# Performance work log

Measured on AMD Instinct MI355X. Metric: run time of the kernel, lower is better.

## Reference

```python
import jax, jax.numpy as jnp
import numpy as np

B, T, C, A, D, H, W = 2, 16, 64, 64, 32, 32, 32  # batch, timepoints, channels, att_features, spatial


def setup_inputs() -> dict:
    key = jax.random.key(0)
    ks = jax.random.split(key, 7)
    s = 1.0 / np.sqrt(C)
    return {
        "x": jax.random.normal(ks[0], (B, T, C, D, H, W), dtype=jnp.float32),
        "Wk": jax.random.normal(ks[1], (A, C), dtype=jnp.float32) * s,
        "bk": jax.random.normal(ks[2], (A,), dtype=jnp.float32) * s,
        "Wq": jax.random.normal(ks[3], (A, C), dtype=jnp.float32) * s,
        "bq": jax.random.normal(ks[4], (A,), dtype=jnp.float32) * s,
        "Wv": jax.random.normal(ks[5], (C, C), dtype=jnp.float32) * s,
        "bv": jax.random.normal(ks[6], (C,), dtype=jnp.float32) * s,
    }


def reference(x, Wk, bk, Wq, bq, Wv, bv):
    # kernel=1 Conv3d == pointwise channel mixing. Project and move spatial
    # dims to the front exactly like movedim((3,4,5),(1,2,3)):
    # result layout [B, D, H, W, T, out_ch].
    def proj(Wt, bt):
        return jnp.einsum('btcdhw,oc->bdhwto', x, Wt) + bt

    k = proj(Wk, bk)  # [B,D,H,W,T,A]
    q = proj(Wq, bq)  # [B,D,H,W,T,A]
    v = proj(Wv, bv)  # [B,D,H,W,T,C]

    scale = 1.0 / np.sqrt(float(Wk.shape[0]))  # sqrt(att_features)
    att = jnp.einsum('bdhwta,bdhwsa->bdhwts', k, q) * scale  # [B,D,H,W,T,T]
    # norm = partial(softmax, dim=1) on the 6-D tensor -> softmax over spatial D axis
    att_map = jax.nn.softmax(att, axis=1)

    # features = (value^T @ att_map)^T: feat[...,s,c] = sum_t v[...,t,c] * att_map[...,t,s]
    feat = jnp.einsum('bdhwtc,bdhwts->bdhwsc', v, att_map)  # [B,D,H,W,T,C]
    # movedim((1,2,3),(3,4,5)): back to [B, T, C, D, H, W]
    return jnp.transpose(feat, (0, 4, 5, 1, 2, 3))
```

## Files before the change

kernel.cpp:

```cpp
#include <hip/hip_runtime.h>

typedef short v8s __attribute__((ext_vector_type(8)));
typedef float v4f __attribute__((ext_vector_type(4)));
typedef float v2f __attribute__((ext_vector_type(2)));

#define NSP 32768
#define ZOFF 8192
#define XSTR 2056
#define FSTR 34

__device__ __forceinline__ unsigned short f2bf(float f) {
  union { float f; unsigned u; } v; v.f = f;
  unsigned r = v.u + 0x7fffu + ((v.u >> 16) & 1u);
  return (unsigned short)(r >> 16);
}
__device__ __forceinline__ unsigned pk(float a, float b) {
  return (unsigned)f2bf(a) | ((unsigned)f2bf(b) << 16);
}

union UF8 { v8s v; unsigned u[4]; uint4 q; };


__global__ __launch_bounds__(512) void prep_kernel(
    const float* __restrict__ Wk, const float* __restrict__ bk,
    const float* __restrict__ Wq, const float* __restrict__ bq,
    const float* __restrict__ Wv, unsigned* __restrict__ ws) {
  __shared__ float sWk[4096], sWq[4096], sWv[4096], sbk[64], sbq[64];
  for (int i = threadIdx.x; i < 4096; i += 512) { sWk[i] = Wk[i]; sWq[i] = Wq[i]; sWv[i] = Wv[i]; }
  if (threadIdx.x < 64) { sbk[threadIdx.x] = bk[threadIdx.x]; sbq[threadIdx.x] = bq[threadIdx.x]; }
  __syncthreads();
  for (int task = threadIdx.x; task < 18 * 64; task += 512) {
    int f = task >> 6, lane = task & 63;
    int i16 = lane & 15, g = lane >> 4;
    unsigned short e[8];
    #pragma unroll
    for (int j = 0; j < 8; ++j) {
      int k = (((j >> 2) << 4) + 4 * g + (j & 3));
      float acc = 0.f;
      if (f < 8) {
        int row = ((f >> 1) << 4) + i16;
        int cc  = ((f & 1) << 5) + k;
        for (int a = 0; a < 64; ++a) acc += sWk[a * 64 + row] * sWq[a * 64 + cc];
      } else if (f < 10) {
        int c = ((f - 8) << 5) + k;
        if (i16 == 0)      { for (int a = 0; a < 64; ++a) acc += sWk[a * 64 + c] * sbq[a]; }
        else if (i16 == 1) { for (int a = 0; a < 64; ++a) acc += sbk[a] * sWq[a * 64 + c]; }
      } else {
        int c  = (((f - 10) >> 1) << 4) + i16;
        int cp = (((f - 10) & 1) << 5) + k;
        acc = sWv[c * 64 + cp];
      }
      e[j] = f2bf(acc);
    }
    unsigned* dst = ws + (size_t)(f * 64 + lane) * 4;
    dst[0] = e[0] | ((unsigned)e[1] << 16);
    dst[1] = e[2] | ((unsigned)e[3] << 16);
    dst[2] = e[4] | ((unsigned)e[5] << 16);
    dst[3] = e[6] | ((unsigned)e[7] << 16);
  }
  if (threadIdx.x == 0) {
    float beta = 0.f;
    for (int a = 0; a < 64; ++a) beta += sbk[a] * sbq[a];
    ((float*)ws)[18 * 256] = beta;
  }
}

#define S2L 0.18033688011112042f

#define DECODE_GRID() \
  int bid = (int)blockIdx.x; \
  int b = bid & 1, dc = (bid >> 1) & 3, h = bid >> 3; \
  const int d0 = dc << 3; \
  const size_t base0 = (size_t)b * 33554432 + h * 32;

#define STAGE_DEFS() \
  const int w2 = tid & 15; \
  const int rp0 = tid >> 4; \
  v2f sA[16], sB[16]; \
  auto issueRegs = [&](int d) { \
    const float* xp = x + base0 + (size_t)d * 1024; \
    _Pragma("unroll") \
    for (int i = 0; i < 16; ++i) { \
      int rp = (i << 5) + rp0; \
      const float* r0 = xp + (size_t)(2 * rp) * NSP + 2 * w2; \
      sA[i] = *(const v2f*)r0; \
      sB[i] = *(const v2f*)(r0 + NSP); \
    } \
  }; \
  auto writeLds = [&]() { \
    _Pragma("unroll") \
    for (int i = 0; i < 16; ++i) { \
      int rp = (i << 5) + rp0; \
      int t = rp >> 5, c = (rp & 31) << 1; \
      int off = (t << 7) + (((c << 1)) ^ ((t & 7) << 4)); \
      *(unsigned*)(&Xbuf[(2 * w2) * XSTR + off])     = pk(sA[i].x, sB[i].x); \
      *(unsigned*)(&Xbuf[(2 * w2 + 1) * XSTR + off]) = pk(sA[i].y, sB[i].y); \
    } \
  };

#define LOADX_DEF() \
  auto loadX = [&](int loc, v8s fX[2]) { \
    const unsigned char* bp = &Xbuf[loc * XSTR + (i16 << 7)]; \
    const int sw = (i16 & 7) << 4; \
    _Pragma("unroll") \
    for (int kc = 0; kc < 2; ++kc) { \
      union { v8s v; unsigned long long dd[2]; } u; \
      int o = (kc << 6) + (g << 3); \
      u.dd[0] = *(const unsigned long long*)(bp + (o ^ sw)); \
      u.dd[1] = *(const unsigned long long*)(bp + ((o + 32) ^ sw)); \
      fX[kc] = u.v; \
    } \
  };

#define ATTOF_DEF() \
  auto attOf = [&](const v8s fX[2]) -> v4f { \
    v4f accW[4]; \
    _Pragma("unroll") \
    for (int tr = 0; tr < 4; ++tr) { \
      v4f a = {0.f, 0.f, 0.f, 0.f}; \
      a = __builtin_amdgcn_mfma_f32_16x16x32_bf16(fM[tr][0], fX[0], a, 0, 0, 0); \
      a = __builtin_amdgcn_mfma_f32_16x16x32_bf16(fM[tr][1], fX[1], a, 0, 0, 0); \
      accW[tr] = a; \
    } \
    v4f au = {0.f, 0.f, 0.f, 0.f}; \
    au = __builtin_amdgcn_mfma_f32_16x16x32_bf16(fUR[0], fX[0], au, 0, 0, 0); \
    au = __builtin_amdgcn_mfma_f32_16x16x32_bf16(fUR[1], fX[1], au, 0, 0, 0); \
    float a1v = au[0] + beta; \
    float a2v = au[1]; \
    float a2s = __shfl(a2v, i16); \
    v4f att; \
    _Pragma("unroll") \
    for (int j = 0; j < 4; ++j) att[j] = __shfl(a1v, 4 * g + j) + a2s; \
    _Pragma("unroll") \
    for (int kc = 0; kc < 2; ++kc) { \
      UF8 w; \
      w.u[0] = pk(accW[2 * kc][0], accW[2 * kc][1]); \
      w.u[1] = pk(accW[2 * kc][2], accW[2 * kc][3]); \
      w.u[2] = pk(accW[2 * kc + 1][0], accW[2 * kc + 1][1]); \
      w.u[3] = pk(accW[2 * kc + 1][2], accW[2 * kc + 1][3]); \
      att = __builtin_amdgcn_mfma_f32_16x16x32_bf16(fX[kc], w.v, att, 0, 0, 0); \
    } \
    return att; \
  };

__global__ __launch_bounds__(512) void pass1_z(
    const float* __restrict__ x, const unsigned* __restrict__ ws,
    float* __restrict__ zp) {
  __shared__ __align__(16) unsigned char Xbuf[32 * XSTR];

  const int tid = (int)threadIdx.x;
  const int lane = tid & 63, wv = tid >> 6;
  const int i16 = lane & 15, g = lane >> 4;
  DECODE_GRID();

  v8s fM[4][2], fUR[2];
  {
    const uint4* W4 = (const uint4*)ws;
    #pragma unroll
    for (int f = 0; f < 8; ++f) { UF8 u; u.q = W4[f * 64 + lane]; fM[f >> 1][f & 1] = u.v; }
    #pragma unroll
    for (int f = 0; f < 2; ++f) { UF8 u; u.q = W4[(8 + f) * 64 + lane]; fUR[f] = u.v; }
  }
  const float beta = ((const float*)ws)[4608];

  STAGE_DEFS();
  LOADX_DEF();
  ATTOF_DEF();

  float Z[4][4] = {};
  issueRegs(d0);
  for (int ii = 0; ii < 8; ++ii) {
    __syncthreads();
    writeLds();
    if (ii < 7) issueRegs(d0 + ii + 1);
    __syncthreads();
    #pragma unroll
    for (int l = 0; l < 4; ++l) {
      v8s fX[2]; loadX(4 * wv + l, fX);
      v4f att = attOf(fX);
      #pragma unroll
      for (int j = 0; j < 4; ++j) Z[l][j] += exp2f(att[j] * S2L);
    }
  }
  const int locg = b * 1024 + h * 32 + 4 * wv;
  #pragma unroll
  for (int l = 0; l < 4; ++l)
    #pragma unroll
    for (int j = 0; j < 4; ++j)
      zp[(((size_t)dc * 2048 + locg + l) << 8) + (4 * g + j) * 16 + i16] = Z[l][j];
}

__global__ __launch_bounds__(512) void pass2_out(
    const float* __restrict__ x, const float* __restrict__ bv,
    const unsigned* __restrict__ ws, const float* __restrict__ zp,
    float* __restrict__ out) {
  __shared__ __align__(16) unsigned char Xbuf[32 * XSTR];
  __shared__ float Fb[512 * FSTR];

  const int tid = (int)threadIdx.x;
  const int lane = tid & 63, wv = tid >> 6;
  const int i16 = lane & 15, g = lane >> 4;
  DECODE_GRID();

  v8s fM[4][2], fUR[2], fWv[4][2];
  {
    const uint4* W4 = (const uint4*)ws;
    #pragma unroll
    for (int f = 0; f < 8; ++f) { UF8 u; u.q = W4[f * 64 + lane]; fM[f >> 1][f & 1] = u.v; }
    #pragma unroll
    for (int f = 0; f < 2; ++f) { UF8 u; u.q = W4[(8 + f) * 64 + lane]; fUR[f] = u.v; }
    #pragma unroll
    for (int f = 0; f < 8; ++f) { UF8 u; u.q = W4[(10 + f) * 64 + lane]; fWv[f >> 1][f & 1] = u.v; }
  }
  const float beta = ((const float*)ws)[4608];
  float bvv[4];
  #pragma unroll
  for (int tn = 0; tn < 4; ++tn) bvv[tn] = bv[i16 + 16 * tn];

  const int locg = b * 1024 + h * 32 + 4 * wv;
  float iZ[4][4];
  #pragma unroll
  for (int l = 0; l < 4; ++l)
    #pragma unroll
    for (int j = 0; j < 4; ++j) {
      float s = 0.f;
      #pragma unroll
      for (int c2 = 0; c2 < 4; ++c2)
        s += zp[(((size_t)c2 * 2048 + locg + l) << 8) + (4 * g + j) * 16 + i16];
      iZ[l][j] = 1.f / s;
    }

  STAGE_DEFS();
  LOADX_DEF();
  ATTOF_DEF();

  auto storeHalf = [&](int half, int d) {
    float* op = out + base0 + (size_t)d * 1024 + ((size_t)half << 5) * NSP;
    const int w4 = tid & 7, rr = tid >> 3;
    #pragma unroll
    for (int ro = 0; ro < 8; ++ro) {
      int r = (ro << 6) + rr;
      int s = r >> 5, ci = r & 31;
      int v = ((r >> 7) & 1) << 2;
      int bse = r * FSTR + ((w4 << 2) ^ v);
      float4 val;
      val.x = Fb[bse]; val.y = Fb[bse + 1]; val.z = Fb[bse + 2]; val.w = Fb[bse + 3];
      *(float4*)(op + (size_t)(s * 64 + ci) * NSP + (w4 << 2)) = val;
    }
  };

  issueRegs(d0 + 7);
  for (int ii = 0; ii < 8; ++ii) {
    const int d = d0 + 7 - ii;
    __syncthreads();
    writeLds();
    if (ii < 7) issueRegs(d - 1);
    __syncthreads();

    unsigned fPs[4][2];
    #pragma unroll
    for (int l = 0; l < 4; ++l) {
      const int w = 4 * wv + l;
      v8s fX[2]; loadX(w, fX);
      v4f att = attOf(fX);
      float p[4];
      #pragma unroll
      for (int j = 0; j < 4; ++j) p[j] = exp2f(att[j] * S2L) * iZ[l][j];
      fPs[l][0] = pk(p[0], p[1]); fPs[l][1] = pk(p[2], p[3]);
      #pragma unroll
      for (int tn = 0; tn < 2; ++tn) {
        v4f a = {bvv[tn], bvv[tn], bvv[tn], bvv[tn]};
        a = __builtin_amdgcn_mfma_f32_16x16x32_bf16(fX[0], fWv[tn][0], a, 0, 0, 0);
        a = __builtin_amdgcn_mfma_f32_16x16x32_bf16(fX[1], fWv[tn][1], a, 0, 0, 0);
        UF8 fV; fV.u[0] = pk(a[0], a[1]); fV.u[1] = pk(a[2], a[3]); fV.u[2] = 0; fV.u[3] = 0;
        UF8 fP; fP.u[0] = fPs[l][0]; fP.u[1] = fPs[l][1]; fP.u[2] = 0; fP.u[3] = 0;
        v4f ft = {0.f, 0.f, 0.f, 0.f};
        ft = __builtin_amdgcn_mfma_f32_16x16x32_bf16(fP.v, fV.v, ft, 0, 0, 0);
        #pragma unroll
        for (int j = 0; j < 4; ++j) {
          int r = (4 * g + j) * 32 + i16 + 16 * tn;
          Fb[r * FSTR + (w ^ (((r >> 7) & 1) << 2))] = ft[j];
        }
      }
    }
    __syncthreads();
    storeHalf(0, d);
    __syncthreads();
    #pragma unroll
    for (int l = 0; l < 4; ++l) {
      const int w = 4 * wv + l;
      v8s fX[2]; loadX(w, fX);
      #pragma unroll
      for (int tn = 2; tn < 4; ++tn) {
        v4f a = {bvv[tn], bvv[tn], bvv[tn], bvv[tn]};
        a = __builtin_amdgcn_mfma_f32_16x16x32_bf16(fX[0], fWv[tn][0], a, 0, 0, 0);
        a = __builtin_amdgcn_mfma_f32_16x16x32_bf16(fX[1], fWv[tn][1], a, 0, 0, 0);
        UF8 fV; fV.u[0] = pk(a[0], a[1]); fV.u[1] = pk(a[2], a[3]); fV.u[2] = 0; fV.u[3] = 0;
        UF8 fP; fP.u[0] = fPs[l][0]; fP.u[1] = fPs[l][1]; fP.u[2] = 0; fP.u[3] = 0;
        v4f ft = {0.f, 0.f, 0.f, 0.f};
        ft = __builtin_amdgcn_mfma_f32_16x16x32_bf16(fP.v, fV.v, ft, 0, 0, 0);
        #pragma unroll
        for (int j = 0; j < 4; ++j) {
          int r = (4 * g + j) * 32 + i16 + 16 * (tn - 2);
          Fb[r * FSTR + (w ^ (((r >> 7) & 1) << 2))] = ft[j];
        }
      }
    }
    __syncthreads();
    storeHalf(1, d);
  }
}

extern "C" void kernel_launch(void* const* d_in, const int* in_sizes, int n_in,
                              void* d_out, int out_size, void* d_ws, size_t ws_size,
                              hipStream_t stream) {
  const float* x  = (const float*)d_in[0];
  const float* Wk = (const float*)d_in[1];
  const float* bk = (const float*)d_in[2];
  const float* Wq = (const float*)d_in[3];
  const float* bq = (const float*)d_in[4];
  const float* Wv = (const float*)d_in[5];
  const float* bv = (const float*)d_in[6];
  float* out = (float*)d_out;
  unsigned* ws = (unsigned*)d_ws;
  float* zp = (float*)d_ws + ZOFF;

  prep_kernel<<<1, 512, 0, stream>>>(Wk, bk, Wq, bq, Wv, ws);
  pass1_z<<<256, 512, 0, stream>>>(x, ws, zp);
  pass2_out<<<256, 512, 0, stream>>>(x, bv, ws, zp, out);
}
```

Baseline: 322.3 us.

## Materialize fp16 logits and bf16 values in pass 1 to avoid recomputing in pass 2

New measurement: 538.8 us. 1.67x slower.

```diff
diff --git a/kernel.cpp b/kernel.cpp
--- a/kernel.cpp
+++ b/kernel.cpp
@@ -1,4 +1,5 @@
 #include <hip/hip_runtime.h>
+#include <hip/hip_fp16.h>
 
 typedef short v8s __attribute__((ext_vector_type(8)));
 typedef float v4f __attribute__((ext_vector_type(4)));
@@ -8,6 +9,12 @@
 #define ZOFF 8192
 #define XSTR 2056
 #define FSTR 34
+#define F2STR 33
+
+#define WS_ZP_B   65536ull
+#define WS_ATT_B  16842752ull
+#define WS_V_B    50397184ull
+#define WS_NEED   184614912ull
 
 __device__ __forceinline__ unsigned short f2bf(float f) {
   union { float f; unsigned u; } v; v.f = f;
@@ -16,6 +23,12 @@
 }
 __device__ __forceinline__ unsigned pk(float a, float b) {
   return (unsigned)f2bf(a) | ((unsigned)f2bf(b) << 16);
+}
+__device__ __forceinline__ unsigned pkh(float a, float b) {
+  union { __half2 h; unsigned u; } c; c.h = __floats2half2_rn(a, b); return c.u;
+}
+__device__ __forceinline__ float2 uph(unsigned u) {
+  union { unsigned u; __half2 h; } c; c.u = u; return __half22float2(c.h);
 }
 
 union UF8 { v8s v; unsigned u[4]; uint4 q; };
@@ -71,6 +84,12 @@
   int bid = (int)blockIdx.x; \
   int b = bid & 1, dc = (bid >> 1) & 3, h = bid >> 3; \
   const int d0 = dc << 3; \
+  const size_t base0 = (size_t)b * 33554432 + h * 32;
+
+#define DECODE512() \
+  int bid = (int)blockIdx.x; \
+  int b = bid & 1, dcc = (bid >> 1) & 7, h = bid >> 4; \
+  const int d0 = dcc << 2; \
   const size_t base0 = (size_t)b * 33554432 + h * 32;
 
 #define STAGE_DEFS() \
@@ -143,16 +162,192 @@
     return att; \
   };
 
+__global__ __launch_bounds__(512, 4) void p1_attv(
+    const float* __restrict__ x, const float* __restrict__ bv,
+    const unsigned* __restrict__ ws, float* __restrict__ zp,
+    unsigned* __restrict__ attw, unsigned* __restrict__ vw) {
+  __shared__ __align__(16) unsigned char Xbuf[32 * XSTR];
+  const int tid = (int)threadIdx.x;
+  const int lane = tid & 63, wv = tid >> 6;
+  const int i16 = lane & 15, g = lane >> 4;
+  DECODE512();
+
+  v8s fM[4][2], fUR[2], fWv[4][2];
+  {
+    const uint4* W4 = (const uint4*)ws;
+    #pragma unroll
+    for (int f = 0; f < 8; ++f) { UF8 u; u.q = W4[f * 64 + lane]; fM[f >> 1][f & 1] = u.v; }
+    #pragma unroll
+    for (int f = 0; f < 2; ++f) { UF8 u; u.q = W4[(8 + f) * 64 + lane]; fUR[f] = u.v; }
+    #pragma unroll
+    for (int f = 0; f < 8; ++f) { UF8 u; u.q = W4[(10 + f) * 64 + lane]; fWv[f >> 1][f & 1] = u.v; }
+  }
+  const float beta = ((const float*)ws)[4608];
+  float bvv[4];
+  #pragma unroll
+  for (int tn = 0; tn < 4; ++tn) bvv[tn] = bv[i16 + 16 * tn];
+
+  STAGE_DEFS();
+  LOADX_DEF();
+  ATTOF_DEF();
+
+  float Z[4][4] = {};
+  issueRegs(d0);
+  for (int ii = 0; ii < 4; ++ii) {
+    __syncthreads();
+    writeLds();
+    if (ii < 3) issueRegs(d0 + ii + 1);
+    __syncthreads();
+    #pragma unroll
+    for (int l = 0; l < 4; ++l) {
+      const int w = 4 * wv + l;
+      const size_t ls = (size_t)(bid * 4 + ii) * 32 + w;
+      v8s fX[2]; loadX(w, fX);
+      v4f att = attOf(fX);
+      float s0 = att[0] * S2L, s1 = att[1] * S2L, s2 = att[2] * S2L, s3 = att[3] * S2L;
+      Z[l][0] += exp2f(s0); Z[l][1] += exp2f(s1);
+      Z[l][2] += exp2f(s2); Z[l][3] += exp2f(s3);
+      uint2 av; av.x = pkh(s0, s1); av.y = pkh(s2, s3);
+      *(uint2*)(attw + ls * 128 + lane * 2) = av;
+      uint4 o0, o1;
+      {
+        v4f a;
+        a = (v4f){bvv[0], bvv[0], bvv[0], bvv[0]};
+        a = __builtin_amdgcn_mfma_f32_16x16x32_bf16(fX[0], fWv[0][0], a, 0, 0, 0);
+        a = __builtin_amdgcn_mfma_f32_16x16x32_bf16(fX[1], fWv[0][1], a, 0, 0, 0);
+        o0.x = pk(a[0], a[1]); o0.y = pk(a[2], a[3]);
+        a = (v4f){bvv[1], bvv[1], bvv[1], bvv[1]};
+        a = __builtin_amdgcn_mfma_f32_16x16x32_bf16(fX[0], fWv[1][0], a, 0, 0, 0);
+        a = __builtin_amdgcn_mfma_f32_16x16x32_bf16(fX[1], fWv[1][1], a, 0, 0, 0);
+        o0.z = pk(a[0], a[1]); o0.w = pk(a[2], a[3]);
+        a = (v4f){bvv[2], bvv[2], bvv[2], bvv[2]};
+        a = __builtin_amdgcn_mfma_f32_16x16x32_bf16(fX[0], fWv[2][0], a, 0, 0, 0);
+        a = __builtin_amdgcn_mfma_f32_16x16x32_bf16(fX[1], fWv[2][1], a, 0, 0, 0);
+        o1.x = pk(a[0], a[1]); o1.y = pk(a[2], a[3]);
+        a = (v4f){bvv[3], bvv[3], bvv[3], bvv[3]};
+        a = __builtin_amdgcn_mfma_f32_16x16x32_bf16(fX[0], fWv[3][0], a, 0, 0, 0);
+        a = __builtin_amdgcn_mfma_f32_16x16x32_bf16(fX[1], fWv[3][1], a, 0, 0, 0);
+        o1.z = pk(a[0], a[1]); o1.w = pk(a[2], a[3]);
+      }
+      uint4* vp = (uint4*)vw + ls * 128 + lane * 2;
+      vp[0] = o0; vp[1] = o1;
+    }
+  }
+  const int locg0 = b * 1024 + h * 32 + 4 * wv;
+  #pragma unroll
+  for (int l = 0; l < 4; ++l)
+    #pragma unroll
+    for (int j = 0; j < 4; ++j)
+      zp[(((size_t)dcc * 2048 + locg0 + l) << 8) + (4 * g + j) * 16 + i16] = Z[l][j];
+}
+
+__global__ __launch_bounds__(512, 4) void p2_feat(
+    const float* __restrict__ zp, const unsigned* __restrict__ attw,
+    const unsigned* __restrict__ vw, float* __restrict__ out) {
+  __shared__ float Fb[512 * F2STR];
+  const int tid = (int)threadIdx.x;
+  const int lane = tid & 63, wv = tid >> 6;
+  const int i16 = lane & 15, g = lane >> 4;
+  DECODE512();
+
+  const int locg0 = b * 1024 + h * 32 + 4 * wv;
+  float iZ[4][4];
+  #pragma unroll
+  for (int l = 0; l < 4; ++l)
+    #pragma unroll
+    for (int j = 0; j < 4; ++j) {
+      float s = 0.f;
+      #pragma unroll
+      for (int c2 = 0; c2 < 8; ++c2)
+        s += zp[(((size_t)c2 * 2048 + locg0 + l) << 8) + (4 * g + j) * 16 + i16];
+      iZ[l][j] = 1.f / s;
+    }
+
+  auto storeHalf = [&](int half, int d) {
+    float* op = out + base0 + (size_t)d * 1024 + ((size_t)half << 5) * NSP;
+    const int w4 = tid & 7, rr = tid >> 3;
+    #pragma unroll
+    for (int ro = 0; ro < 8; ++ro) {
+      int r = (ro << 6) + rr;
+      int s = r >> 5, ci = r & 31;
+      int col = (w4 << 2) ^ (((r >> 7) & 1) << 4);
+      int bse = r * F2STR + col;
+      float4 val;
+      val.x = Fb[bse]; val.y = Fb[bse + 1]; val.z = Fb[bse + 2]; val.w = Fb[bse + 3];
+      *(float4*)(op + (size_t)(s * 64 + ci) * NSP + (w4 << 2)) = val;
+    }
+  };
+
+  for (int ii = 0; ii < 4; ++ii) {
+    const int d = d0 + ii;
+    uint2 ar[4]; uint4 va[4], vb[4];
+    #pragma unroll
+    for (int l = 0; l < 4; ++l) {
+      const size_t ls = (size_t)(bid * 4 + ii) * 32 + 4 * wv + l;
+      ar[l] = *(const uint2*)(attw + ls * 128 + lane * 2);
+      const uint4* vp = (const uint4*)vw + ls * 128 + lane * 2;
+      va[l] = vp[0]; vb[l] = vp[1];
+    }
+    unsigned fPu[4][2];
+    __syncthreads();
+    #pragma unroll
+    for (int l = 0; l < 4; ++l) {
+      const int w = 4 * wv + l;
+      float2 f01 = uph(ar[l].x), f23 = uph(ar[l].y);
+      float p0 = exp2f(f01.x) * iZ[l][0], p1 = exp2f(f01.y) * iZ[l][1];
+      float p2 = exp2f(f23.x) * iZ[l][2], p3 = exp2f(f23.y) * iZ[l][3];
+      fPu[l][0] = pk(p0, p1); fPu[l][1] = pk(p2, p3);
+      UF8 fP; fP.u[0] = fPu[l][0]; fP.u[1] = fPu[l][1]; fP.u[2] = 0; fP.u[3] = 0;
+      #pragma unroll
+      for (int tn = 0; tn < 2; ++tn) {
+        UF8 fV;
+        fV.u[0] = tn == 0 ? va[l].x : va[l].z;
+        fV.u[1] = tn == 0 ? va[l].y : va[l].w;
+        fV.u[2] = 0; fV.u[3] = 0;
+        v4f ft = {0.f, 0.f, 0.f, 0.f};
+        ft = __builtin_amdgcn_mfma_f32_16x16x32_bf16(fP.v, fV.v, ft, 0, 0, 0);
+        #pragma unroll
+        for (int j = 0; j < 4; ++j) {
+          int r = (4 * g + j) * 32 + i16 + 16 * tn;
+          Fb[r * F2STR + (w ^ ((g & 1) << 4))] = ft[j];
+        }
+      }
+    }
+    __syncthreads();
+    storeHalf(0, d);
+    __syncthreads();
+    #pragma unroll
+    for (int l = 0; l < 4; ++l) {
+      const int w = 4 * wv + l;
+      UF8 fP; fP.u[0] = fPu[l][0]; fP.u[1] = fPu[l][1]; fP.u[2] = 0; fP.u[3] = 0;
+      #pragma unroll
+      for (int tn = 0; tn < 2; ++tn) {
+        UF8 fV;
+        fV.u[0] = tn == 0 ? vb[l].x : vb[l].z;
+        fV.u[1] = tn == 0 ? vb[l].y : vb[l].w;
+        fV.u[2] = 0; fV.u[3] = 0;
+        v4f ft = {0.f, 0.f, 0.f, 0.f};
+        ft = __builtin_amdgcn_mfma_f32_16x16x32_bf16(fP.v, fV.v, ft, 0, 0, 0);
+        #pragma unroll
+        for (int j = 0; j < 4; ++j) {
+          int r = (4 * g + j) * 32 + i16 + 16 * tn;
+          Fb[r * F2STR + (w ^ ((g & 1) << 4))] = ft[j];
+        }
+      }
+    }
+    __syncthreads();
+    storeHalf(1, d);
+  }
+}
+
 __global__ __launch_bounds__(512) void pass1_z(
     const float* __restrict__ x, const unsigned* __restrict__ ws,
     float* __restrict__ zp) {
   __shared__ __align__(16) unsigned char Xbuf[32 * XSTR];
-
   const int tid = (int)threadIdx.x;
   const int lane = tid & 63, wv = tid >> 6;
   const int i16 = lane & 15, g = lane >> 4;
   DECODE_GRID();
-
   v8s fM[4][2], fUR[2];
   {
     const uint4* W4 = (const uint4*)ws;
@@ -162,11 +357,7 @@
     for (int f = 0; f < 2; ++f) { UF8 u; u.q = W4[(8 + f) * 64 + lane]; fUR[f] = u.v; }
   }
   const float beta = ((const float*)ws)[4608];
-
-  STAGE_DEFS();
-  LOADX_DEF();
-  ATTOF_DEF();
-
+  STAGE_DEFS(); LOADX_DEF(); ATTOF_DEF();
   float Z[4][4] = {};
   issueRegs(d0);
   for (int ii = 0; ii < 8; ++ii) {
@@ -196,12 +387,10 @@
     float* __restrict__ out) {
   __shared__ __align__(16) unsigned char Xbuf[32 * XSTR];
   __shared__ float Fb[512 * FSTR];
-
   const int tid = (int)threadIdx.x;
   const int lane = tid & 63, wv = tid >> 6;
   const int i16 = lane & 15, g = lane >> 4;
   DECODE_GRID();
-
   v8s fM[4][2], fUR[2], fWv[4][2];
   {
     const uint4* W4 = (const uint4*)ws;
@@ -216,7 +405,6 @@
   float bvv[4];
   #pragma unroll
   for (int tn = 0; tn < 4; ++tn) bvv[tn] = bv[i16 + 16 * tn];
-
   const int locg = b * 1024 + h * 32 + 4 * wv;
   float iZ[4][4];
   #pragma unroll
@@ -229,11 +417,7 @@
         s += zp[(((size_t)c2 * 2048 + locg + l) << 8) + (4 * g + j) * 16 + i16];
       iZ[l][j] = 1.f / s;
     }
-
-  STAGE_DEFS();
-  LOADX_DEF();
-  ATTOF_DEF();
-
+  STAGE_DEFS(); LOADX_DEF(); ATTOF_DEF();
   auto storeHalf = [&](int half, int d) {
     float* op = out + base0 + (size_t)d * 1024 + ((size_t)half << 5) * NSP;
     const int w4 = tid & 7, rr = tid >> 3;
@@ -248,7 +432,6 @@
       *(float4*)(op + (size_t)(s * 64 + ci) * NSP + (w4 << 2)) = val;
     }
   };
-
   issueRegs(d0 + 7);
   for (int ii = 0; ii < 8; ++ii) {
     const int d = d0 + 7 - ii;
@@ -256,7 +439,6 @@
     writeLds();
     if (ii < 7) issueRegs(d - 1);
     __syncthreads();
-
     unsigned fPs[4][2];
     #pragma unroll
     for (int l = 0; l < 4; ++l) {
@@ -323,9 +505,17 @@
   const float* bv = (const float*)d_in[6];
   float* out = (float*)d_out;
   unsigned* ws = (unsigned*)d_ws;
-  float* zp = (float*)d_ws + ZOFF;
 
   prep_kernel<<<1, 512, 0, stream>>>(Wk, bk, Wq, bq, Wv, ws);
-  pass1_z<<<256, 512, 0, stream>>>(x, ws, zp);
-  pass2_out<<<256, 512, 0, stream>>>(x, bv, ws, zp, out);
-}
+  if (ws_size >= WS_NEED) {
+    float*    zp   = (float*)((char*)d_ws + WS_ZP_B);
+    unsigned* attw = (unsigned*)((char*)d_ws + WS_ATT_B);
+    unsigned* vw   = (unsigned*)((char*)d_ws + WS_V_B);
+    p1_attv<<<512, 512, 0, stream>>>(x, bv, ws, zp, attw, vw);
+    p2_feat<<<512, 512, 0, stream>>>(zp, attw, vw, out);
+  } else {
+    float* zp = (float*)d_ws + ZOFF;
+    pass1_z<<<256, 512, 0, stream>>>(x, ws, zp);
+    pass2_out<<<256, 512, 0, stream>>>(x, bv, ws, zp, out);
+  }
+}
```

## Double grid to 512 blocks, drop register prefetch, shrink LDS for higher occupancy

Applied to the files above, without the earlier changes.

Result: slower. 556.7 us (+72.7%).

```diff
diff --git a/kernel.cpp b/kernel.cpp
--- a/kernel.cpp
+++ b/kernel.cpp
@@ -5,9 +5,9 @@
 typedef float v2f __attribute__((ext_vector_type(2)));
 
 #define NSP 32768
-#define ZOFF 8192
 #define XSTR 2056
-#define FSTR 34
+#define FSTR 17
+#define WS_ZP_B 65536ull
 
 __device__ __forceinline__ unsigned short f2bf(float f) {
   union { float f; unsigned u; } v; v.f = f;
@@ -67,36 +67,11 @@
 
 #define S2L 0.18033688011112042f
 
-#define DECODE_GRID() \
+#define DECODE512() \
   int bid = (int)blockIdx.x; \
-  int b = bid & 1, dc = (bid >> 1) & 3, h = bid >> 3; \
-  const int d0 = dc << 3; \
+  int b = bid & 1, dcc = (bid >> 1) & 7, h = bid >> 4; \
+  const int d0 = dcc << 2; \
   const size_t base0 = (size_t)b * 33554432 + h * 32;
-
-#define STAGE_DEFS() \
-  const int w2 = tid & 15; \
-  const int rp0 = tid >> 4; \
-  v2f sA[16], sB[16]; \
-  auto issueRegs = [&](int d) { \
-    const float* xp = x + base0 + (size_t)d * 1024; \
-    _Pragma("unroll") \
-    for (int i = 0; i < 16; ++i) { \
-      int rp = (i << 5) + rp0; \
-      const float* r0 = xp + (size_t)(2 * rp) * NSP + 2 * w2; \
-      sA[i] = *(const v2f*)r0; \
-      sB[i] = *(const v2f*)(r0 + NSP); \
-    } \
-  }; \
-  auto writeLds = [&]() { \
-    _Pragma("unroll") \
-    for (int i = 0; i < 16; ++i) { \
-      int rp = (i << 5) + rp0; \
-      int t = rp >> 5, c = (rp & 31) << 1; \
-      int off = (t << 7) + (((c << 1)) ^ ((t & 7) << 4)); \
-      *(unsigned*)(&Xbuf[(2 * w2) * XSTR + off])     = pk(sA[i].x, sB[i].x); \
-      *(unsigned*)(&Xbuf[(2 * w2 + 1) * XSTR + off]) = pk(sA[i].y, sB[i].y); \
-    } \
-  };
 
 #define LOADX_DEF() \
   auto loadX = [&](int loc, v8s fX[2]) { \
@@ -143,15 +118,14 @@
     return att; \
   };
 
-__global__ __launch_bounds__(512) void pass1_z(
+__global__ __launch_bounds__(512, 4) void pass1_z(
     const float* __restrict__ x, const unsigned* __restrict__ ws,
     float* __restrict__ zp) {
   __shared__ __align__(16) unsigned char Xbuf[32 * XSTR];
-
   const int tid = (int)threadIdx.x;
   const int lane = tid & 63, wv = tid >> 6;
   const int i16 = lane & 15, g = lane >> 4;
-  DECODE_GRID();
+  DECODE512();
 
   v8s fM[4][2], fUR[2];
   {
@@ -163,16 +137,35 @@
   }
   const float beta = ((const float*)ws)[4608];
 
-  STAGE_DEFS();
+  const int w2 = tid & 15;
+  const int rp0 = tid >> 4;
   LOADX_DEF();
   ATTOF_DEF();
 
   float Z[4][4] = {};
-  issueRegs(d0);
-  for (int ii = 0; ii < 8; ++ii) {
+  for (int ii = 0; ii < 4; ++ii) {
+    const int d = d0 + ii;
     __syncthreads();
-    writeLds();
-    if (ii < 7) issueRegs(d0 + ii + 1);
+    const float* xp = x + base0 + (size_t)d * 1024;
+    #pragma unroll
+    for (int ch = 0; ch < 2; ++ch) {
+      v2f sA[8], sB[8];
+      #pragma unroll
+      for (int i = 0; i < 8; ++i) {
+        int rp = ((ch * 8 + i) << 5) + rp0;
+        const float* r0 = xp + (size_t)(2 * rp) * NSP + 2 * w2;
+        sA[i] = *(const v2f*)r0;
+        sB[i] = *(const v2f*)(r0 + NSP);
+      }
+      #pragma unroll
+      for (int i = 0; i < 8; ++i) {
+        int rp = ((ch * 8 + i) << 5) + rp0;
+        int t = rp >> 5, c = (rp & 31) << 1;
+        int off = (t << 7) + (((c << 1)) ^ ((t & 7) << 4));
+        *(unsigned*)(&Xbuf[(2 * w2) * XSTR + off])     = pk(sA[i].x, sB[i].x);
+        *(unsigned*)(&Xbuf[(2 * w2 + 1) * XSTR + off]) = pk(sA[i].y, sB[i].y);
+      }
+    }
     __syncthreads();
     #pragma unroll
     for (int l = 0; l < 4; ++l) {
@@ -187,127 +180,164 @@
   for (int l = 0; l < 4; ++l)
     #pragma unroll
     for (int j = 0; j < 4; ++j)
-      zp[(((size_t)dc * 2048 + locg + l) << 8) + (4 * g + j) * 16 + i16] = Z[l][j];
-}
-
-__global__ __launch_bounds__(512) void pass2_out(
+      zp[(((size_t)dcc * 2048 + locg + l) << 8) + (4 * g + j) * 16 + i16] = Z[l][j];
+}
+
+__global__ __launch_bounds__(512, 4) void pass2_out(
     const float* __restrict__ x, const float* __restrict__ bv,
     const unsigned* __restrict__ ws, const float* __restrict__ zp,
     float* __restrict__ out) {
-  __shared__ __align__(16) unsigned char Xbuf[32 * XSTR];
+  __shared__ __align__(16) unsigned char Xbuf[16 * XSTR];
   __shared__ float Fb[512 * FSTR];
+  __shared__ unsigned Wvs[2048];
 
   const int tid = (int)threadIdx.x;
   const int lane = tid & 63, wv = tid >> 6;
   const int i16 = lane & 15, g = lane >> 4;
-  DECODE_GRID();
-
-  v8s fM[4][2], fUR[2], fWv[4][2];
+  DECODE512();
+
+  v8s fM[4][2], fUR[2];
   {
     const uint4* W4 = (const uint4*)ws;
     #pragma unroll
     for (int f = 0; f < 8; ++f) { UF8 u; u.q = W4[f * 64 + lane]; fM[f >> 1][f & 1] = u.v; }
     #pragma unroll
     for (int f = 0; f < 2; ++f) { UF8 u; u.q = W4[(8 + f) * 64 + lane]; fUR[f] = u.v; }
-    #pragma unroll
-    for (int f = 0; f < 8; ++f) { UF8 u; u.q = W4[(10 + f) * 64 + lane]; fWv[f >> 1][f & 1] = u.v; }
   }
   const float beta = ((const float*)ws)[4608];
   float bvv[4];
   #pragma unroll
   for (int tn = 0; tn < 4; ++tn) bvv[tn] = bv[i16 + 16 * tn];
 
-  const int locg = b * 1024 + h * 32 + 4 * wv;
+  for (int o = tid; o < 2048; o += 512) {
+    int r = o & 255, L = r >> 2, dd = r & 3;
+    Wvs[(o & ~255) + ((dd >> 1) << 7) + 2 * L + (dd & 1)] = ws[2560 + o];
+  }
+
   float iZ[4][4];
   #pragma unroll
-  for (int l = 0; l < 4; ++l)
+  for (int q = 0; q < 4; ++q) {
+    int w = ((q >> 1) << 4) + 2 * wv + (q & 1);
+    int locg = b * 1024 + h * 32 + w;
     #pragma unroll
     for (int j = 0; j < 4; ++j) {
       float s = 0.f;
       #pragma unroll
-      for (int c2 = 0; c2 < 4; ++c2)
-        s += zp[(((size_t)c2 * 2048 + locg + l) << 8) + (4 * g + j) * 16 + i16];
-      iZ[l][j] = 1.f / s;
-    }
-
-  STAGE_DEFS();
+      for (int c2 = 0; c2 < 8; ++c2)
+        s += zp[(((size_t)c2 * 2048 + locg) << 8) + (4 * g + j) * 16 + i16];
+      iZ[q][j] = 1.f / s;
+    }
+  }
+
+  const int w2h = tid & 7;
+  const int rp0 = tid >> 3;
   LOADX_DEF();
   ATTOF_DEF();
 
-  auto storeHalf = [&](int half, int d) {
-    float* op = out + base0 + (size_t)d * 1024 + ((size_t)half << 5) * NSP;
-    const int w4 = tid & 7, rr = tid >> 3;
-    #pragma unroll
-    for (int ro = 0; ro < 8; ++ro) {
-      int r = (ro << 6) + rr;
-      int s = r >> 5, ci = r & 31;
-      int v = ((r >> 7) & 1) << 2;
-      int bse = r * FSTR + ((w4 << 2) ^ v);
+  auto loadWv = [&](int tn, int kc) -> v8s {
+    int base = ((tn * 2 + kc) << 8) + 2 * lane;
+    union { v8s v; unsigned long long dd[2]; } u;
+    u.dd[0] = *(const unsigned long long*)&Wvs[base];
+    u.dd[1] = *(const unsigned long long*)&Wvs[base + 128];
+    return u.v;
+  };
+
+  auto storeFb = [&](int cHalf, int d, int wh) {
+    float* op = out + base0 + (size_t)d * 1024 + wh * 16 + (size_t)cHalf * 32 * NSP;
+    const int q = tid & 3, rr = tid >> 2;
+    #pragma unroll
+    for (int it = 0; it < 4; ++it) {
+      int r = (it << 7) + rr;
+      int gg = (r >> 7) & 3;
+      const float* fp = &Fb[r * FSTR + 4 * q];
       float4 val;
-      val.x = Fb[bse]; val.y = Fb[bse + 1]; val.z = Fb[bse + 2]; val.w = Fb[bse + 3];
-      *(float4*)(op + (size_t)(s * 64 + ci) * NSP + (w4 << 2)) = val;
+      val.x = fp[0 ^ gg]; val.y = fp[1 ^ gg]; val.z = fp[2 ^ gg]; val.w = fp[3 ^ gg];
+      *(float4*)(op + (size_t)((r >> 5) * 64 + (r & 31)) * NSP + 4 * q) = val;
     }
   };
 
-  issueRegs(d0 + 7);
-  for (int ii = 0; ii < 8; ++ii) {
-    const int d = d0 + 7 - ii;
-    __syncthreads();
-    writeLds();
-    if (ii < 7) issueRegs(d - 1);
-    __syncthreads();
-
-    unsigned fPs[4][2];
-    #pragma unroll
-    for (int l = 0; l < 4; ++l) {
-      const int w = 4 * wv + l;
-      v8s fX[2]; loadX(w, fX);
-      v4f att = attOf(fX);
-      float p[4];
-      #pragma unroll
-      for (int j = 0; j < 4; ++j) p[j] = exp2f(att[j] * S2L) * iZ[l][j];
-      fPs[l][0] = pk(p[0], p[1]); fPs[l][1] = pk(p[2], p[3]);
-      #pragma unroll
-      for (int tn = 0; tn < 2; ++tn) {
-        v4f a = {bvv[tn], bvv[tn], bvv[tn], bvv[tn]};
-        a = __builtin_amdgcn_mfma_f32_16x16x32_bf16(fX[0], fWv[tn][0], a, 0, 0, 0);
-        a = __builtin_amdgcn_mfma_f32_16x16x32_bf16(fX[1], fWv[tn][1], a, 0, 0, 0);
-        UF8 fV; fV.u[0] = pk(a[0], a[1]); fV.u[1] = pk(a[2], a[3]); fV.u[2] = 0; fV.u[3] = 0;
-        UF8 fP; fP.u[0] = fPs[l][0]; fP.u[1] = fPs[l][1]; fP.u[2] = 0; fP.u[3] = 0;
-        v4f ft = {0.f, 0.f, 0.f, 0.f};
-        ft = __builtin_amdgcn_mfma_f32_16x16x32_bf16(fP.v, fV.v, ft, 0, 0, 0);
-        #pragma unroll
-        for (int j = 0; j < 4; ++j) {
-          int r = (4 * g + j) * 32 + i16 + 16 * tn;
-          Fb[r * FSTR + (w ^ (((r >> 7) & 1) << 2))] = ft[j];
+  __syncthreads();
+
+  for (int ii = 0; ii < 4; ++ii) {
+    const int d = d0 + ii;
+    #pragma unroll
+    for (int wh = 0; wh < 2; ++wh) {
+      const float* xp = x + base0 + (size_t)d * 1024 + wh * 16;
+      #pragma unroll
+      for (int ch = 0; ch < 2; ++ch) {
+        v2f sA[4], sB[4];
+        #pragma unroll
+        for (int i = 0; i < 4; ++i) {
+          int rp = ((ch * 4 + i) << 6) + rp0;
+          const float* r0 = xp + (size_t)(2 * rp) * NSP + 2 * w2h;
+          sA[i] = *(const v2f*)r0;
+          sB[i] = *(const v2f*)(r0 + NSP);
         }
-      }
-    }
-    __syncthreads();
-    storeHalf(0, d);
-    __syncthreads();
-    #pragma unroll
-    for (int l = 0; l < 4; ++l) {
-      const int w = 4 * wv + l;
-      v8s fX[2]; loadX(w, fX);
-      #pragma unroll
-      for (int tn = 2; tn < 4; ++tn) {
-        v4f a = {bvv[tn], bvv[tn], bvv[tn], bvv[tn]};
-        a = __builtin_amdgcn_mfma_f32_16x16x32_bf16(fX[0], fWv[tn][0], a, 0, 0, 0);
-        a = __builtin_amdgcn_mfma_f32_16x16x32_bf16(fX[1], fWv[tn][1], a, 0, 0, 0);
-        UF8 fV; fV.u[0] = pk(a[0], a[1]); fV.u[1] = pk(a[2], a[3]); fV.u[2] = 0; fV.u[3] = 0;
-        UF8 fP; fP.u[0] = fPs[l][0]; fP.u[1] = fPs[l][1]; fP.u[2] = 0; fP.u[3] = 0;
-        v4f ft = {0.f, 0.f, 0.f, 0.f};
-        ft = __builtin_amdgcn_mfma_f32_16x16x32_bf16(fP.v, fV.v, ft, 0, 0, 0);
-        #pragma unroll
-        for (int j = 0; j < 4; ++j) {
-          int r = (4 * g + j) * 32 + i16 + 16 * (tn - 2);
-          Fb[r * FSTR + (w ^ (((r >> 7) & 1) << 2))] = ft[j];
+        #pragma unroll
+        for (int i = 0; i < 4; ++i) {
+          int rp = ((ch * 4 + i) << 6) + rp0;
+          int t = rp >> 5, c = (rp & 31) << 1;
+          int off = (t << 7) + (((c << 1)) ^ ((t & 7) << 4));
+          *(unsigned*)(&Xbuf[(2 * w2h) * XSTR + off])     = pk(sA[i].x, sB[i].x);
+          *(unsigned*)(&Xbuf[(2 * w2h + 1) * XSTR + off]) = pk(sA[i].y, sB[i].y);
         }
       }
-    }
-    __syncthreads();
-    storeHalf(1, d);
+      __syncthreads();
+      unsigned fPs[2][2];
+      #pragma unroll
+      for (int l = 0; l < 2; ++l) {
+        const int wp = 2 * wv + l;
+        v8s fX[2]; loadX(wp, fX);
+        v4f att = attOf(fX);
+        const int q = wh * 2 + l;
+        float p[4];
+        #pragma unroll
+        for (int j = 0; j < 4; ++j) p[j] = exp2f(att[j] * S2L) * iZ[q][j];
+        fPs[l][0] = pk(p[0], p[1]); fPs[l][1] = pk(p[2], p[3]);
+        #pragma unroll
+        for (int tn = 0; tn < 2; ++tn) {
+          v8s w0 = loadWv(tn, 0), w1 = loadWv(tn, 1);
+          v4f a = {bvv[tn], bvv[tn], bvv[tn], bvv[tn]};
+          a = __builtin_amdgcn_mfma_f32_16x16x32_bf16(fX[0], w0, a, 0, 0, 0);
+          a = __builtin_amdgcn_mfma_f32_16x16x32_bf16(fX[1], w1, a, 0, 0, 0);
+          UF8 fV; fV.u[0] = pk(a[0], a[1]); fV.u[1] = pk(a[2], a[3]); fV.u[2] = 0; fV.u[3] = 0;
+          UF8 fP; fP.u[0] = fPs[l][0]; fP.u[1] = fPs[l][1]; fP.u[2] = 0; fP.u[3] = 0;
+          v4f ft = {0.f, 0.f, 0.f, 0.f};
+          ft = __builtin_amdgcn_mfma_f32_16x16x32_bf16(fP.v, fV.v, ft, 0, 0, 0);
+          #pragma unroll
+          for (int j = 0; j < 4; ++j) {
+            int r = (4 * g + j) * 32 + i16 + 16 * tn;
+            Fb[r * FSTR + (wp ^ g)] = ft[j];
+          }
+        }
+      }
+      __syncthreads();
+      storeFb(0, d, wh);
+      __syncthreads();
+      #pragma unroll
+      for (int l = 0; l < 2; ++l) {
+        const int wp = 2 * wv + l;
+        v8s fX[2]; loadX(wp, fX);
+        #pragma unroll
+        for (int tn = 2; tn < 4; ++tn) {
+          v8s w0 = loadWv(tn, 0), w1 = loadWv(tn, 1);
+          v4f a = {bvv[tn], bvv[tn], bvv[tn], bvv[tn]};
+          a = __builtin_amdgcn_mfma_f32_16x16x32_bf16(fX[0], w0, a, 0, 0, 0);
+          a = __builtin_amdgcn_mfma_f32_16x16x32_bf16(fX[1], w1, a, 0, 0, 0);
+          UF8 fV; fV.u[0] = pk(a[0], a[1]); fV.u[1] = pk(a[2], a[3]); fV.u[2] = 0; fV.u[3] = 0;
+          UF8 fP; fP.u[0] = fPs[l][0]; fP.u[1] = fPs[l][1]; fP.u[2] = 0; fP.u[3] = 0;
+          v4f ft = {0.f, 0.f, 0.f, 0.f};
+          ft = __builtin_amdgcn_mfma_f32_16x16x32_bf16(fP.v, fV.v, ft, 0, 0, 0);
+          #pragma unroll
+          for (int j = 0; j < 4; ++j) {
+            int r = (4 * g + j) * 32 + i16 + 16 * (tn - 2);
+            Fb[r * FSTR + (wp ^ g)] = ft[j];
+          }
+        }
+      }
+      __syncthreads();
+      storeFb(1, d, wh);
+    }
   }
 }
 
@@ -323,9 +353,9 @@
   const float* bv = (const float*)d_in[6];
   float* out = (float*)d_out;
   unsigned* ws = (unsigned*)d_ws;
-  float* zp = (float*)d_ws + ZOFF;
+  float* zp = (float*)((char*)d_ws + WS_ZP_B);
 
   prep_kernel<<<1, 512, 0, stream>>>(Wk, bk, Wq, bq, Wv, ws);
-  pass1_z<<<256, 512, 0, stream>>>(x, ws, zp);
-  pass2_out<<<256, 512, 0, stream>>>(x, bv, ws, zp, out);
-}
+  pass1_z<<<512, 512, 0, stream>>>(x, ws, zp);
+  pass2_out<<<512, 512, 0, stream>>>(x, bv, ws, zp, out);
+}
```

## Double block size to 1024 threads and move Wv fragments into LDS

Applied to the files above, without the earlier changes.

Measured after the change: 543.5 us. 1.69x slower.

```diff
diff --git a/kernel.cpp b/kernel.cpp
--- a/kernel.cpp
+++ b/kernel.cpp
@@ -5,9 +5,9 @@
 typedef float v2f __attribute__((ext_vector_type(2)));
 
 #define NSP 32768
-#define ZOFF 8192
 #define XSTR 2056
 #define FSTR 34
+#define WS_ZP_B 65536ull
 
 __device__ __forceinline__ unsigned short f2bf(float f) {
   union { float f; unsigned u; } v; v.f = f;
@@ -76,12 +76,12 @@
 #define STAGE_DEFS() \
   const int w2 = tid & 15; \
   const int rp0 = tid >> 4; \
-  v2f sA[16], sB[16]; \
+  v2f sA[8], sB[8]; \
   auto issueRegs = [&](int d) { \
     const float* xp = x + base0 + (size_t)d * 1024; \
     _Pragma("unroll") \
-    for (int i = 0; i < 16; ++i) { \
-      int rp = (i << 5) + rp0; \
+    for (int i = 0; i < 8; ++i) { \
+      int rp = (i << 6) + rp0; \
       const float* r0 = xp + (size_t)(2 * rp) * NSP + 2 * w2; \
       sA[i] = *(const v2f*)r0; \
       sB[i] = *(const v2f*)(r0 + NSP); \
@@ -89,8 +89,8 @@
   }; \
   auto writeLds = [&]() { \
     _Pragma("unroll") \
-    for (int i = 0; i < 16; ++i) { \
-      int rp = (i << 5) + rp0; \
+    for (int i = 0; i < 8; ++i) { \
+      int rp = (i << 6) + rp0; \
       int t = rp >> 5, c = (rp & 31) << 1; \
       int off = (t << 7) + (((c << 1)) ^ ((t & 7) << 4)); \
       *(unsigned*)(&Xbuf[(2 * w2) * XSTR + off])     = pk(sA[i].x, sB[i].x); \
@@ -143,11 +143,10 @@
     return att; \
   };
 
-__global__ __launch_bounds__(512) void pass1_z(
+__global__ __launch_bounds__(1024) void pass1_z(
     const float* __restrict__ x, const unsigned* __restrict__ ws,
     float* __restrict__ zp) {
   __shared__ __align__(16) unsigned char Xbuf[32 * XSTR];
-
   const int tid = (int)threadIdx.x;
   const int lane = tid & 63, wv = tid >> 6;
   const int i16 = lane & 15, g = lane >> 4;
@@ -167,7 +166,7 @@
   LOADX_DEF();
   ATTOF_DEF();
 
-  float Z[4][4] = {};
+  float Z[2][4] = {};
   issueRegs(d0);
   for (int ii = 0; ii < 8; ++ii) {
     __syncthreads();
@@ -175,77 +174,90 @@
     if (ii < 7) issueRegs(d0 + ii + 1);
     __syncthreads();
     #pragma unroll
-    for (int l = 0; l < 4; ++l) {
-      v8s fX[2]; loadX(4 * wv + l, fX);
+    for (int l = 0; l < 2; ++l) {
+      v8s fX[2]; loadX(2 * wv + l, fX);
       v4f att = attOf(fX);
       #pragma unroll
       for (int j = 0; j < 4; ++j) Z[l][j] += exp2f(att[j] * S2L);
     }
   }
-  const int locg = b * 1024 + h * 32 + 4 * wv;
   #pragma unroll
-  for (int l = 0; l < 4; ++l)
+  for (int l = 0; l < 2; ++l) {
+    const int locg = b * 1024 + h * 32 + 2 * wv + l;
     #pragma unroll
     for (int j = 0; j < 4; ++j)
-      zp[(((size_t)dc * 2048 + locg + l) << 8) + (4 * g + j) * 16 + i16] = Z[l][j];
-}
-
-__global__ __launch_bounds__(512) void pass2_out(
+      zp[(((size_t)dc * 2048 + locg) << 8) + (4 * g + j) * 16 + i16] = Z[l][j];
+  }
+}
+
+__global__ __launch_bounds__(1024) void pass2_out(
     const float* __restrict__ x, const float* __restrict__ bv,
     const unsigned* __restrict__ ws, const float* __restrict__ zp,
     float* __restrict__ out) {
   __shared__ __align__(16) unsigned char Xbuf[32 * XSTR];
   __shared__ float Fb[512 * FSTR];
+  __shared__ unsigned Wvs[2048];
 
   const int tid = (int)threadIdx.x;
   const int lane = tid & 63, wv = tid >> 6;
   const int i16 = lane & 15, g = lane >> 4;
   DECODE_GRID();
 
-  v8s fM[4][2], fUR[2], fWv[4][2];
+  v8s fM[4][2], fUR[2];
   {
     const uint4* W4 = (const uint4*)ws;
     #pragma unroll
     for (int f = 0; f < 8; ++f) { UF8 u; u.q = W4[f * 64 + lane]; fM[f >> 1][f & 1] = u.v; }
     #pragma unroll
     for (int f = 0; f < 2; ++f) { UF8 u; u.q = W4[(8 + f) * 64 + lane]; fUR[f] = u.v; }
-    #pragma unroll
-    for (int f = 0; f < 8; ++f) { UF8 u; u.q = W4[(10 + f) * 64 + lane]; fWv[f >> 1][f & 1] = u.v; }
   }
   const float beta = ((const float*)ws)[4608];
   float bvv[4];
   #pragma unroll
   for (int tn = 0; tn < 4; ++tn) bvv[tn] = bv[i16 + 16 * tn];
 
-  const int locg = b * 1024 + h * 32 + 4 * wv;
-  float iZ[4][4];
+  for (int o = tid; o < 2048; o += 1024) {
+    int r = o & 255, L = r >> 2, dd = r & 3;
+    Wvs[(o & ~255) + ((dd >> 1) << 7) + 2 * L + (dd & 1)] = ws[2560 + o];
+  }
+
+  float iZ[2][4];
   #pragma unroll
-  for (int l = 0; l < 4; ++l)
+  for (int l = 0; l < 2; ++l) {
+    const int locg = b * 1024 + h * 32 + 2 * wv + l;
     #pragma unroll
     for (int j = 0; j < 4; ++j) {
       float s = 0.f;
       #pragma unroll
       for (int c2 = 0; c2 < 4; ++c2)
-        s += zp[(((size_t)c2 * 2048 + locg + l) << 8) + (4 * g + j) * 16 + i16];
+        s += zp[(((size_t)c2 * 2048 + locg) << 8) + (4 * g + j) * 16 + i16];
       iZ[l][j] = 1.f / s;
     }
+  }
 
   STAGE_DEFS();
   LOADX_DEF();
   ATTOF_DEF();
 
+  auto loadWv = [&](int tn, int kc) -> v8s {
+    int base = ((tn * 2 + kc) << 8) + 2 * lane;
+    union { v8s v; unsigned long long dd[2]; } u;
+    u.dd[0] = *(const unsigned long long*)&Wvs[base];
+    u.dd[1] = *(const unsigned long long*)&Wvs[base + 128];
+    return u.v;
+  };
+
   auto storeHalf = [&](int half, int d) {
     float* op = out + base0 + (size_t)d * 1024 + ((size_t)half << 5) * NSP;
     const int w4 = tid & 7, rr = tid >> 3;
     #pragma unroll
-    for (int ro = 0; ro < 8; ++ro) {
-      int r = (ro << 6) + rr;
-      int s = r >> 5, ci = r & 31;
+    for (int it = 0; it < 4; ++it) {
+      int r = (it << 7) + rr;
       int v = ((r >> 7) & 1) << 2;
       int bse = r * FSTR + ((w4 << 2) ^ v);
       float4 val;
       val.x = Fb[bse]; val.y = Fb[bse + 1]; val.z = Fb[bse + 2]; val.w = Fb[bse + 3];
-      *(float4*)(op + (size_t)(s * 64 + ci) * NSP + (w4 << 2)) = val;
+      *(float4*)(op + (size_t)((r >> 5) * 64 + (r & 31)) * NSP + (w4 << 2)) = val;
     }
   };
 
@@ -257,11 +269,11 @@
     if (ii < 7) issueRegs(d - 1);
     __syncthreads();
 
-    unsigned fPs[4][2];
-    #pragma unroll
-    for (int l = 0; l < 4; ++l) {
-      const int w = 4 * wv + l;
-      v8s fX[2]; loadX(w, fX);
+    unsigned fPs[2][2];
+    #pragma unroll
+    for (int l = 0; l < 2; ++l) {
+      const int wp = 2 * wv + l;
+      v8s fX[2]; loadX(wp, fX);
       v4f att = attOf(fX);
       float p[4];
       #pragma unroll
@@ -269,9 +281,10 @@
       fPs[l][0] = pk(p[0], p[1]); fPs[l][1] = pk(p[2], p[3]);
       #pragma unroll
       for (int tn = 0; tn < 2; ++tn) {
+        v8s w0 = loadWv(tn, 0), w1 = loadWv(tn, 1);
         v4f a = {bvv[tn], bvv[tn], bvv[tn], bvv[tn]};
-        a = __builtin_amdgcn_mfma_f32_16x16x32_bf16(fX[0], fWv[tn][0], a, 0, 0, 0);
-        a = __builtin_amdgcn_mfma_f32_16x16x32_bf16(fX[1], fWv[tn][1], a, 0, 0, 0);
+        a = __builtin_amdgcn_mfma_f32_16x16x32_bf16(fX[0], w0, a, 0, 0, 0);
+        a = __builtin_amdgcn_mfma_f32_16x16x32_bf16(fX[1], w1, a, 0, 0, 0);
         UF8 fV; fV.u[0] = pk(a[0], a[1]); fV.u[1] = pk(a[2], a[3]); fV.u[2] = 0; fV.u[3] = 0;
         UF8 fP; fP.u[0] = fPs[l][0]; fP.u[1] = fPs[l][1]; fP.u[2] = 0; fP.u[3] = 0;
         v4f ft = {0.f, 0.f, 0.f, 0.f};
@@ -279,7 +292,7 @@
         #pragma unroll
         for (int j = 0; j < 4; ++j) {
           int r = (4 * g + j) * 32 + i16 + 16 * tn;
-          Fb[r * FSTR + (w ^ (((r >> 7) & 1) << 2))] = ft[j];
+          Fb[r * FSTR + (wp ^ (((r >> 7) & 1) << 2))] = ft[j];
         }
       }
     }
@@ -287,14 +300,15 @@
     storeHalf(0, d);
     __syncthreads();
     #pragma unroll
-    for (int l = 0; l < 4; ++l) {
-      const int w = 4 * wv + l;
-      v8s fX[2]; loadX(w, fX);
+    for (int l = 0; l < 2; ++l) {
+      const int wp = 2 * wv + l;
+      v8s fX[2]; loadX(wp, fX);
       #pragma unroll
       for (int tn = 2; tn < 4; ++tn) {
+        v8s w0 = loadWv(tn, 0), w1 = loadWv(tn, 1);
         v4f a = {bvv[tn], bvv[tn], bvv[tn], bvv[tn]};
-        a = __builtin_amdgcn_mfma_f32_16x16x32_bf16(fX[0], fWv[tn][0], a, 0, 0, 0);
-        a = __builtin_amdgcn_mfma_f32_16x16x32_bf16(fX[1], fWv[tn][1], a, 0, 0, 0);
+        a = __builtin_amdgcn_mfma_f32_16x16x32_bf16(fX[0], w0, a, 0, 0, 0);
+        a = __builtin_amdgcn_mfma_f32_16x16x32_bf16(fX[1], w1, a, 0, 0, 0);
         UF8 fV; fV.u[0] = pk(a[0], a[1]); fV.u[1] = pk(a[2], a[3]); fV.u[2] = 0; fV.u[3] = 0;
         UF8 fP; fP.u[0] = fPs[l][0]; fP.u[1] = fPs[l][1]; fP.u[2] = 0; fP.u[3] = 0;
         v4f ft = {0.f, 0.f, 0.f, 0.f};
@@ -302,7 +316,7 @@
         #pragma unroll
         for (int j = 0; j < 4; ++j) {
           int r = (4 * g + j) * 32 + i16 + 16 * (tn - 2);
-          Fb[r * FSTR + (w ^ (((r >> 7) & 1) << 2))] = ft[j];
+          Fb[r * FSTR + (wp ^ (((r >> 7) & 1) << 2))] = ft[j];
         }
       }
     }
@@ -323,9 +337,9 @@
   const float* bv = (const float*)d_in[6];
   float* out = (float*)d_out;
   unsigned* ws = (unsigned*)d_ws;
-  float* zp = (float*)d_ws + ZOFF;
+  float* zp = (float*)((char*)d_ws + WS_ZP_B);
 
   prep_kernel<<<1, 512, 0, stream>>>(Wk, bk, Wq, bq, Wv, ws);
-  pass1_z<<<256, 512, 0, stream>>>(x, ws, zp);
-  pass2_out<<<256, 512, 0, stream>>>(x, bv, ws, zp, out);
-}
+  pass1_z<<<256, 1024, 0, stream>>>(x, ws, zp);
+  pass2_out<<<256, 1024, 0, stream>>>(x, bv, ws, zp, out);
+}
```
